# Kernel tuning notes

Measured on AMD Instinct MI355X. Metric: run time of the kernel, lower is better.

The kernel has to match this reference:

```python
import jax, jax.numpy as jnp
import numpy as np

N, E = 50000, 250000          # nodes, edges
IN, OUT, EDIM = 9, 84, 1      # NNConv(9, 84), edge nn Linear(1, 9*84)
EPS = 1e-5                    # BatchNorm1d default eps


def setup_inputs() -> dict:
    key = jax.random.key(0)
    ks = jax.random.split(key, 8)
    return {
        "x": jax.random.normal(ks[0], (N, IN), jnp.float32),
        "edge_index": jax.random.randint(ks[1], (2, E), 0, N, dtype=jnp.int64),
        "edge_attr": jax.random.normal(ks[2], (E, EDIM), jnp.float32),
        # edge nn: Linear(EDIM, IN*OUT) generating per-edge weight matrices
        "nn_w": jax.random.normal(ks[3], (EDIM, IN * OUT), jnp.float32) * (1.0 / np.sqrt(EDIM)),
        "nn_b": jnp.zeros((IN * OUT,), jnp.float32),
        # NNConv root weight + bias
        "root": jax.random.normal(ks[4], (IN, OUT), jnp.float32) * (1.0 / np.sqrt(IN)),
        "bias": jnp.zeros((OUT,), jnp.float32),
        # BatchNorm1d(84) affine params
        "gamma": jnp.ones((OUT,), jnp.float32),
        "beta": jnp.zeros((OUT,), jnp.float32),
    }


def reference(x, edge_index, edge_attr, nn_w, nn_b, root, bias, gamma, beta):
    src, dst = edge_index[0], edge_index[1]
    # per-edge weight matrices: [E, IN, OUT]
    w_e = (edge_attr @ nn_w + nn_b).reshape(E, IN, OUT)
    # gather source node features and apply edge-specific matmul: [E, OUT]
    msg = jnp.einsum('ei,eio->eo', x[src], w_e)
    # scatter-add to destination nodes (NNConv default aggr='add'): [N, OUT]
    aggr = jax.ops.segment_sum(msg, dst, num_segments=N)
    out = x @ root + aggr + bias
    # BatchNorm1d(84), training mode (biased batch stats)
    mean = out.mean(0)
    var = out.var(0)
    out = (out - mean) * jax.lax.rsqrt(var + EPS) * gamma + beta
    return out
```

## Files before the change

kernel.cpp:

```cpp
#include <hip/hip_runtime.h>

#define N_NODES 50000
#define E_EDGES 250000
#define IN_F 9
#define OUT_F 84
#define GROUPS 21
#define BN_EPS 1e-5f

#define NB_TILE 24
#define NTILES ((N_NODES + NB_TILE - 1) / NB_TILE)
#define NCOPIES 32
#define CAP 32

#define CNT_OFF   0
#define STATC_OFF 50048
#define SLOT_OFF  55552

__global__ void fill_slots_kernel(const int* __restrict__ ei,
                                  const float* __restrict__ ea,
                                  int* __restrict__ cnt,
                                  int2* __restrict__ slot,
                                  float* __restrict__ statc) {
    if (blockIdx.x == 0) {
        for (int t = threadIdx.x; t < NCOPIES * 2 * OUT_F; t += blockDim.x)
            statc[t] = 0.0f;
    }
    int e = blockIdx.x * blockDim.x + threadIdx.x;
    if (e < E_EDGES) {
        int dst = ei[E_EDGES + e];
        int pos = atomicAdd(&cnt[dst], 1);
        if (pos < CAP)
            slot[dst * CAP + pos] = make_int2(ei[e], __float_as_int(ea[e]));
    }
}

__global__ void fused_kernel(const float* __restrict__ x,
                             const float* __restrict__ nw,
                             const float* __restrict__ nb,
                             const float* __restrict__ root,
                             const float* __restrict__ bias,
                             const int*   __restrict__ cnt,
                             const int2*  __restrict__ slot,
                             float* __restrict__ out,
                             float* __restrict__ statc) {
    __shared__ __align__(16) float4 Ws[IN_F * GROUPS];
    __shared__ __align__(16) float4 Bs[IN_F * GROUPS];
    __shared__ __align__(16) float4 Rs[IN_F * GROUPS];
    __shared__ __align__(16) float4 bs4[GROUPS];
    __shared__ float Stile[NB_TILE * 18];
    __shared__ float Xtile[NB_TILE * IN_F];
    __shared__ float sbin[2 * OUT_F];

    const int tid = threadIdx.x;
    for (int t = tid; t < IN_F * GROUPS; t += blockDim.x) {
        Ws[t] = ((const float4*)nw)[t];
        Bs[t] = ((const float4*)nb)[t];
        Rs[t] = ((const float4*)root)[t];
    }
    if (tid < GROUPS) bs4[tid] = ((const float4*)bias)[tid];
    if (tid < 2 * OUT_F) sbin[tid] = 0.0f;

    const int nbase = blockIdx.x * NB_TILE;

    if (tid < NB_TILE * IN_F) {
        int nl = tid / IN_F, i = tid - nl * IN_F;
        int n = nbase + nl;
        float s0 = 0.f, s1 = 0.f;
        if (n < N_NODES) {
            Xtile[nl * IN_F + i] = x[n * IN_F + i];
            int c = cnt[n];
            if (c > CAP) c = CAP;
            const int2* row = &slot[n * CAP];
            int k = 0;
            for (; k + 2 <= c; k += 2) {
                int2 r0 = row[k], r1 = row[k + 1];
                float xv0 = x[r0.x * IN_F + i];
                float xv1 = x[r1.x * IN_F + i];
                s0 += xv0 + xv1;
                s1 += __int_as_float(r0.y) * xv0 + __int_as_float(r1.y) * xv1;
            }
            if (k < c) {
                int2 r0 = row[k];
                float xv0 = x[r0.x * IN_F + i];
                s0 += xv0;
                s1 += __int_as_float(r0.y) * xv0;
            }
        }
        Stile[nl * 18 + i]     = s0;
        Stile[nl * 18 + 9 + i] = s1;
    }
    __syncthreads();

    float4 sa = make_float4(0.f, 0.f, 0.f, 0.f);
    float4 qa = make_float4(0.f, 0.f, 0.f, 0.f);
    const int g = tid % GROUPS;
    if (tid < 252) {
#pragma unroll
        for (int k = 0; k < 2; ++k) {
            int p  = tid + k * 252;
            int nl = p / GROUPS;
            int n  = nbase + nl;
            if (n < N_NODES) {
                float4 acc = bs4[g];
#pragma unroll
                for (int i = 0; i < IN_F; ++i) {
                    float xv = Xtile[nl * IN_F + i];
                    float s0 = Stile[nl * 18 + i];
                    float s1 = Stile[nl * 18 + 9 + i];
                    float4 r = Rs[i * GROUPS + g];
                    float4 w = Ws[i * GROUPS + g];
                    float4 b = Bs[i * GROUPS + g];
                    acc.x += xv * r.x + s1 * w.x + s0 * b.x;
                    acc.y += xv * r.y + s1 * w.y + s0 * b.y;
                    acc.z += xv * r.z + s1 * w.z + s0 * b.z;
                    acc.w += xv * r.w + s1 * w.w + s0 * b.w;
                }
                *(float4*)&out[n * OUT_F + g * 4] = acc;
                sa.x += acc.x; sa.y += acc.y; sa.z += acc.z; sa.w += acc.w;
                qa.x += acc.x * acc.x; qa.y += acc.y * acc.y;
                qa.z += acc.z * acc.z; qa.w += acc.w * acc.w;
            }
        }
        atomicAdd(&sbin[g * 4 + 0], sa.x);
        atomicAdd(&sbin[g * 4 + 1], sa.y);
        atomicAdd(&sbin[g * 4 + 2], sa.z);
        atomicAdd(&sbin[g * 4 + 3], sa.w);
        atomicAdd(&sbin[OUT_F + g * 4 + 0], qa.x);
        atomicAdd(&sbin[OUT_F + g * 4 + 1], qa.y);
        atomicAdd(&sbin[OUT_F + g * 4 + 2], qa.z);
        atomicAdd(&sbin[OUT_F + g * 4 + 3], qa.w);
    }
    __syncthreads();
    float* sc = statc + (blockIdx.x & (NCOPIES - 1)) * (2 * OUT_F);
    if (tid < 2 * OUT_F) atomicAdd(&sc[tid], sbin[tid]);
}

__global__ void norm_kernel(float* __restrict__ out,
                            const float* __restrict__ statc,
                            const float* __restrict__ gamma,
                            const float* __restrict__ beta) {
    __shared__ float scale[OUT_F];
    __shared__ float shift[OUT_F];
    __shared__ float red[2 * OUT_F];

    const int tid = threadIdx.x;
    if (tid < 2 * OUT_F) {
        float acc = 0.0f;
#pragma unroll
        for (int c = 0; c < NCOPIES; ++c)
            acc += statc[c * (2 * OUT_F) + tid];
        red[tid] = acc;
    }
    __syncthreads();
    if (tid < OUT_F) {
        const float inv_n = 1.0f / (float)N_NODES;
        float m   = red[tid] * inv_n;
        float var = red[OUT_F + tid] * inv_n - m * m;
        float sc  = rsqrtf(var + BN_EPS) * gamma[tid];
        scale[tid] = sc;
        shift[tid] = beta[tid] - m * sc;
    }
    __syncthreads();

    int gid = blockIdx.x * blockDim.x + tid;
    if (gid >= N_NODES * GROUPS) return;
    int g = gid % GROUPS;

    float4 v = ((float4*)out)[gid];
    v.x = v.x * scale[g * 4 + 0] + shift[g * 4 + 0];
    v.y = v.y * scale[g * 4 + 1] + shift[g * 4 + 1];
    v.z = v.z * scale[g * 4 + 2] + shift[g * 4 + 2];
    v.w = v.w * scale[g * 4 + 3] + shift[g * 4 + 3];
    ((float4*)out)[gid] = v;
}

extern "C" void kernel_launch(void* const* d_in, const int* in_sizes, int n_in,
                              void* d_out, int out_size, void* d_ws, size_t ws_size,
                              hipStream_t stream) {
    const float* x     = (const float*)d_in[0];
    const int*   ei    = (const int*)d_in[1];
    const float* ea    = (const float*)d_in[2];
    const float* nw    = (const float*)d_in[3];
    const float* nb    = (const float*)d_in[4];
    const float* root  = (const float*)d_in[5];
    const float* bias  = (const float*)d_in[6];
    const float* gamma = (const float*)d_in[7];
    const float* beta  = (const float*)d_in[8];
    float*       out   = (float*)d_out;

    float* wsf   = (float*)d_ws;
    int*   wsi   = (int*)d_ws;
    int*   cnt   = wsi + CNT_OFF;
    float* statc = wsf + STATC_OFF;
    int2*  slot  = (int2*)(wsi + SLOT_OFF);

    hipMemsetAsync(cnt, 0, N_NODES * sizeof(int), stream);
    fill_slots_kernel<<<(E_EDGES + 255) / 256, 256, 0, stream>>>(ei, ea, cnt, slot, statc);
    fused_kernel<<<NTILES, 256, 0, stream>>>(x, nw, nb, root, bias,
                                             cnt, slot, out, statc);
    norm_kernel<<<(N_NODES * GROUPS + 255) / 256, 256, 0, stream>>>(out, statc, gamma, beta);
}
```

Baseline: 135.4 us.

## Compute BatchNorm stats from Gram matrix of node features before output write

```diff
diff --git a/kernel.cpp b/kernel.cpp
--- a/kernel.cpp
+++ b/kernel.cpp
@@ -12,9 +12,15 @@
 #define NCOPIES 32
 #define CAP 32
 
+#define VDIM 27
+#define NPAIR 378
+#define NM 405
+#define SLEN 408
+
 #define CNT_OFF   0
 #define STATC_OFF 50048
-#define SLOT_OFF  55552
+#define SLOT_OFF  63232
+#define S_OFF     3263232
 
 __global__ void fill_slots_kernel(const int* __restrict__ ei,
                                   const float* __restrict__ ea,
@@ -22,7 +28,7 @@
                                   int2* __restrict__ slot,
                                   float* __restrict__ statc) {
     if (blockIdx.x == 0) {
-        for (int t = threadIdx.x; t < NCOPIES * 2 * OUT_F; t += blockDim.x)
+        for (int t = threadIdx.x; t < NCOPIES * SLEN; t += blockDim.x)
             statc[t] = 0.0f;
     }
     int e = blockIdx.x * blockDim.x + threadIdx.x;
@@ -34,67 +40,160 @@
     }
 }
 
-__global__ void fused_kernel(const float* __restrict__ x,
-                             const float* __restrict__ nw,
-                             const float* __restrict__ nb,
-                             const float* __restrict__ root,
-                             const float* __restrict__ bias,
-                             const int*   __restrict__ cnt,
-                             const int2*  __restrict__ slot,
-                             float* __restrict__ out,
-                             float* __restrict__ statc) {
-    __shared__ __align__(16) float4 Ws[IN_F * GROUPS];
-    __shared__ __align__(16) float4 Bs[IN_F * GROUPS];
-    __shared__ __align__(16) float4 Rs[IN_F * GROUPS];
-    __shared__ __align__(16) float4 bs4[GROUPS];
-    __shared__ float Stile[NB_TILE * 18];
-    __shared__ float Xtile[NB_TILE * IN_F];
-    __shared__ float sbin[2 * OUT_F];
+__global__ void gather_gram_kernel(const float* __restrict__ x,
+                                   const int*   __restrict__ cnt,
+                                   const int2*  __restrict__ slot,
+                                   float* __restrict__ S,
+                                   float* __restrict__ statc) {
+    __shared__ float V[VDIM * (NB_TILE + 1)];
+    __shared__ unsigned char pI[NPAIR], pJ[NPAIR];
 
     const int tid = threadIdx.x;
-    for (int t = tid; t < IN_F * GROUPS; t += blockDim.x) {
-        Ws[t] = ((const float4*)nw)[t];
-        Bs[t] = ((const float4*)nb)[t];
-        Rs[t] = ((const float4*)root)[t];
-    }
-    if (tid < GROUPS) bs4[tid] = ((const float4*)bias)[tid];
-    if (tid < 2 * OUT_F) sbin[tid] = 0.0f;
+
+    for (int t = tid; t < NPAIR; t += blockDim.x) {
+        int tt = t, i = 0;
+        while (tt >= VDIM - i) { tt -= VDIM - i; ++i; }
+        pI[t] = (unsigned char)i;
+        pJ[t] = (unsigned char)(i + tt);
+    }
 
     const int nbase = blockIdx.x * NB_TILE;
 
     if (tid < NB_TILE * IN_F) {
         int nl = tid / IN_F, i = tid - nl * IN_F;
         int n = nbase + nl;
-        float s0 = 0.f, s1 = 0.f;
+        float xv = 0.f, s0 = 0.f, s1 = 0.f;
         if (n < N_NODES) {
-            Xtile[nl * IN_F + i] = x[n * IN_F + i];
+            xv = x[n * IN_F + i];
             int c = cnt[n];
             if (c > CAP) c = CAP;
             const int2* row = &slot[n * CAP];
             int k = 0;
             for (; k + 2 <= c; k += 2) {
                 int2 r0 = row[k], r1 = row[k + 1];
-                float xv0 = x[r0.x * IN_F + i];
-                float xv1 = x[r1.x * IN_F + i];
-                s0 += xv0 + xv1;
-                s1 += __int_as_float(r0.y) * xv0 + __int_as_float(r1.y) * xv1;
+                float a0 = x[r0.x * IN_F + i];
+                float a1 = x[r1.x * IN_F + i];
+                s0 += a0 + a1;
+                s1 += __int_as_float(r0.y) * a0 + __int_as_float(r1.y) * a1;
             }
             if (k < c) {
                 int2 r0 = row[k];
-                float xv0 = x[r0.x * IN_F + i];
-                s0 += xv0;
-                s1 += __int_as_float(r0.y) * xv0;
+                float a0 = x[r0.x * IN_F + i];
+                s0 += a0;
+                s1 += __int_as_float(r0.y) * a0;
             }
-        }
-        Stile[nl * 18 + i]     = s0;
-        Stile[nl * 18 + 9 + i] = s1;
+            S[n * 18 + i]     = s0;
+            S[n * 18 + 9 + i] = s1;
+        }
+        V[i * (NB_TILE + 1) + nl]            = xv;
+        V[(9 + i) * (NB_TILE + 1) + nl]      = s0;
+        V[(18 + i) * (NB_TILE + 1) + nl]     = s1;
     }
     __syncthreads();
 
-    float4 sa = make_float4(0.f, 0.f, 0.f, 0.f);
-    float4 qa = make_float4(0.f, 0.f, 0.f, 0.f);
+    float* sc = statc + (blockIdx.x & (NCOPIES - 1)) * SLEN;
+    for (int t = tid; t < NM; t += blockDim.x) {
+        float acc = 0.f;
+        if (t < NPAIR) {
+            const float* vi = &V[pI[t] * (NB_TILE + 1)];
+            const float* vj = &V[pJ[t] * (NB_TILE + 1)];
+#pragma unroll
+            for (int n = 0; n < NB_TILE; ++n) acc += vi[n] * vj[n];
+        } else {
+            const float* vi = &V[(t - NPAIR) * (NB_TILE + 1)];
+#pragma unroll
+            for (int n = 0; n < NB_TILE; ++n) acc += vi[n];
+        }
+        atomicAdd(&sc[t], acc);
+    }
+}
+
+__global__ void final_kernel(const float* __restrict__ x,
+                             const float* __restrict__ S,
+                             const float* __restrict__ nw,
+                             const float* __restrict__ nb,
+                             const float* __restrict__ root,
+                             const float* __restrict__ bias,
+                             const float* __restrict__ gamma,
+                             const float* __restrict__ beta,
+                             const float* __restrict__ statc,
+                             float* __restrict__ out) {
+    __shared__ __align__(16) float4 Ws[IN_F * GROUPS];
+    __shared__ __align__(16) float4 Bs[IN_F * GROUPS];
+    __shared__ __align__(16) float4 Rs[IN_F * GROUPS];
+    __shared__ __align__(16) float4 bs4[GROUPS];
+    __shared__ float M[NM];
+    __shared__ __align__(16) float scale[OUT_F];
+    __shared__ __align__(16) float shift[OUT_F];
+    __shared__ float Xt[NB_TILE * IN_F];
+    __shared__ float St[NB_TILE * 18];
+
+    const int tid = threadIdx.x;
+    const int nbase = blockIdx.x * NB_TILE;
+
+    for (int t = tid; t < IN_F * GROUPS; t += blockDim.x) {
+        Ws[t] = ((const float4*)nw)[t];
+        Bs[t] = ((const float4*)nb)[t];
+        Rs[t] = ((const float4*)root)[t];
+    }
+    if (tid < GROUPS) bs4[tid] = ((const float4*)bias)[tid];
+
+    if (tid < NB_TILE * IN_F) {
+        int nl = tid / IN_F, i = tid - nl * IN_F;
+        int n = nbase + nl;
+        float xv = 0.f, s0 = 0.f, s1 = 0.f;
+        if (n < N_NODES) {
+            xv = x[n * IN_F + i];
+            s0 = S[n * 18 + i];
+            s1 = S[n * 18 + 9 + i];
+        }
+        Xt[nl * IN_F + i]  = xv;
+        St[nl * 18 + i]     = s0;
+        St[nl * 18 + 9 + i] = s1;
+    }
+
+    for (int t = tid; t < NM; t += blockDim.x) {
+        float a = 0.f;
+#pragma unroll
+        for (int c = 0; c < NCOPIES; ++c) a += statc[c * SLEN + t];
+        M[t] = a;
+    }
+    __syncthreads();
+
+    if (tid < OUT_F) {
+        const int o = tid;
+        float c[VDIM];
+#pragma unroll
+        for (int i = 0; i < IN_F; ++i) {
+            c[i]      = root[i * OUT_F + o];
+            c[9 + i]  = nb[i * OUT_F + o];
+            c[18 + i] = nw[i * OUT_F + o];
+        }
+        float sv = 0.f;
+#pragma unroll
+        for (int i = 0; i < VDIM; ++i) sv += M[NPAIR + i] * c[i];
+        float q = 0.f;
+        int t2 = 0;
+        for (int i = 0; i < VDIM; ++i) {
+            q += c[i] * c[i] * M[t2++];
+            for (int j = i + 1; j < VDIM; ++j)
+                q += 2.f * c[i] * c[j] * M[t2++];
+        }
+        const float b = bias[o];
+        const float inv_n = 1.0f / (float)N_NODES;
+        float mean  = (sv + (float)N_NODES * b) * inv_n;
+        float sumsq = q + 2.f * b * sv + (float)N_NODES * b * b;
+        float var   = sumsq * inv_n - mean * mean;
+        float sc    = rsqrtf(var + BN_EPS) * gamma[o];
+        scale[o] = sc;
+        shift[o] = beta[o] - mean * sc;
+    }
+    __syncthreads();
+
     const int g = tid % GROUPS;
     if (tid < 252) {
+        float4 sc4 = *(const float4*)&scale[g * 4];
+        float4 sh4 = *(const float4*)&shift[g * 4];
 #pragma unroll
         for (int k = 0; k < 2; ++k) {
             int p  = tid + k * 252;
@@ -104,9 +203,9 @@
                 float4 acc = bs4[g];
 #pragma unroll
                 for (int i = 0; i < IN_F; ++i) {
-                    float xv = Xtile[nl * IN_F + i];
-                    float s0 = Stile[nl * 18 + i];
-                    float s1 = Stile[nl * 18 + 9 + i];
+                    float xv = Xt[nl * IN_F + i];
+                    float s0 = St[nl * 18 + i];
+                    float s1 = St[nl * 18 + 9 + i];
                     float4 r = Rs[i * GROUPS + g];
                     float4 w = Ws[i * GROUPS + g];
                     float4 b = Bs[i * GROUPS + g];
@@ -115,63 +214,14 @@
                     acc.z += xv * r.z + s1 * w.z + s0 * b.z;
                     acc.w += xv * r.w + s1 * w.w + s0 * b.w;
                 }
+                acc.x = acc.x * sc4.x + sh4.x;
+                acc.y = acc.y * sc4.y + sh4.y;
+                acc.z = acc.z * sc4.z + sh4.z;
+                acc.w = acc.w * sc4.w + sh4.w;
                 *(float4*)&out[n * OUT_F + g * 4] = acc;
-                sa.x += acc.x; sa.y += acc.y; sa.z += acc.z; sa.w += acc.w;
-                qa.x += acc.x * acc.x; qa.y += acc.y * acc.y;
-                qa.z += acc.z * acc.z; qa.w += acc.w * acc.w;
             }
         }
-        atomicAdd(&sbin[g * 4 + 0], sa.x);
-        atomicAdd(&sbin[g * 4 + 1], sa.y);
-        atomicAdd(&sbin[g * 4 + 2], sa.z);
-        atomicAdd(&sbin[g * 4 + 3], sa.w);
-        atomicAdd(&sbin[OUT_F + g * 4 + 0], qa.x);
-        atomicAdd(&sbin[OUT_F + g * 4 + 1], qa.y);
-        atomicAdd(&sbin[OUT_F + g * 4 + 2], qa.z);
-        atomicAdd(&sbin[OUT_F + g * 4 + 3], qa.w);
-    }
-    __syncthreads();
-    float* sc = statc + (blockIdx.x & (NCOPIES - 1)) * (2 * OUT_F);
-    if (tid < 2 * OUT_F) atomicAdd(&sc[tid], sbin[tid]);
-}
-
-__global__ void norm_kernel(float* __restrict__ out,
-                            const float* __restrict__ statc,
-                            const float* __restrict__ gamma,
-                            const float* __restrict__ beta) {
-    __shared__ float scale[OUT_F];
-    __shared__ float shift[OUT_F];
-    __shared__ float red[2 * OUT_F];
-
-    const int tid = threadIdx.x;
-    if (tid < 2 * OUT_F) {
-        float acc = 0.0f;
-#pragma unroll
-        for (int c = 0; c < NCOPIES; ++c)
-            acc += statc[c * (2 * OUT_F) + tid];
-        red[tid] = acc;
-    }
-    __syncthreads();
-    if (tid < OUT_F) {
-        const float inv_n = 1.0f / (float)N_NODES;
-        float m   = red[tid] * inv_n;
-        float var = red[OUT_F + tid] * inv_n - m * m;
-        float sc  = rsqrtf(var + BN_EPS) * gamma[tid];
-        scale[tid] = sc;
-        shift[tid] = beta[tid] - m * sc;
-    }
-    __syncthreads();
-
-    int gid = blockIdx.x * blockDim.x + tid;
-    if (gid >= N_NODES * GROUPS) return;
-    int g = gid % GROUPS;
-
-    float4 v = ((float4*)out)[gid];
-    v.x = v.x * scale[g * 4 + 0] + shift[g * 4 + 0];
-    v.y = v.y * scale[g * 4 + 1] + shift[g * 4 + 1];
-    v.z = v.z * scale[g * 4 + 2] + shift[g * 4 + 2];
-    v.w = v.w * scale[g * 4 + 3] + shift[g * 4 + 3];
-    ((float4*)out)[gid] = v;
+    }
 }
 
 extern "C" void kernel_launch(void* const* d_in, const int* in_sizes, int n_in,
@@ -193,10 +243,11 @@
     int*   cnt   = wsi + CNT_OFF;
     float* statc = wsf + STATC_OFF;
     int2*  slot  = (int2*)(wsi + SLOT_OFF);
+    float* S     = wsf + S_OFF;
 
     hipMemsetAsync(cnt, 0, N_NODES * sizeof(int), stream);
     fill_slots_kernel<<<(E_EDGES + 255) / 256, 256, 0, stream>>>(ei, ea, cnt, slot, statc);
-    fused_kernel<<<NTILES, 256, 0, stream>>>(x, nw, nb, root, bias,
-                                             cnt, slot, out, statc);
-    norm_kernel<<<(N_NODES * GROUPS + 255) / 256, 256, 0, stream>>>(out, statc, gamma, beta);
-}
+    gather_gram_kernel<<<NTILES, 256, 0, stream>>>(x, cnt, slot, S, statc);
+    final_kernel<<<NTILES, 256, 0, stream>>>(x, S, nw, nb, root, bias,
+                                             gamma, beta, statc, out);
+}
```

Result: faster. 124.8 us (-7.8%).
